# Kernel tuning notes

Hardware: AMD Instinct MI355X
Metric: run time of the kernel (lower is better)

Reference implementation:

```python
import jax, jax.numpy as jnp
import numpy as np
from itertools import product

MAX_ALLOC = [3, 3, 3, 3, 3, 3]   # env.maximum_allocation -> 4^6 = 4096 actions
NUM_SESSIONS = 64
STATE_DIM = NUM_SESSIONS + len(MAX_ALLOC)  # 70
HIDDEN = (1024, 1024)
BATCH = 8192


def setup_inputs() -> dict:
    key = jax.random.key(0)
    ks = jax.random.split(key, 8)
    # states: sessions part uniform [0,1); waitlist part uniform [0,4) so mask is nontrivial
    sessions = jax.random.uniform(ks[0], (BATCH, NUM_SESSIONS), dtype=jnp.float32)
    waitlist = jax.random.uniform(ks[1], (BATCH, len(MAX_ALLOC)), dtype=jnp.float32) * 4.0
    states = jnp.concatenate([sessions, waitlist], axis=1)
    # enumerated action space, same order as itertools.product in the torch module
    action_space = jnp.asarray(
        np.array(list(product(*[range(m + 1) for m in MAX_ALLOC])), dtype=np.int32))  # [4096, 6]
    A = action_space.shape[0]
    W1 = jax.random.normal(ks[2], (STATE_DIM, HIDDEN[0]), dtype=jnp.float32) / np.sqrt(STATE_DIM)
    b1 = jnp.zeros((HIDDEN[0],), dtype=jnp.float32)
    W2 = jax.random.normal(ks[3], (HIDDEN[0], HIDDEN[1]), dtype=jnp.float32) / np.sqrt(HIDDEN[0])
    b2 = jnp.zeros((HIDDEN[1],), dtype=jnp.float32)
    Wh = jax.random.normal(ks[4], (HIDDEN[1], A), dtype=jnp.float32) / np.sqrt(HIDDEN[1])
    bh = jnp.zeros((A,), dtype=jnp.float32)
    return {"states": states, "W1": W1, "b1": b1, "W2": W2, "b2": b2,
            "Wh": Wh, "bh": bh, "action_space": action_space,
            "num_sessions": NUM_SESSIONS}


def reference(states, W1, b1, W2, b2, Wh, bh, action_space, num_sessions):
    # vectorized get_action_mask: action j is feasible for row i iff all(action_j <= waitlist_i)
    waitlist = states[:, num_sessions:]                                   # [B, 6]
    feasible = jnp.all(action_space[None, :, :].astype(states.dtype)
                       <= waitlist[:, None, :], axis=-1)                  # [B, A] bool
    mask = feasible.astype(states.dtype)
    # tanh MLP
    h = jnp.tanh(states @ W1 + b1)
    h = jnp.tanh(h @ W2 + b2)
    logits = h @ Wh + bh + jnp.log(mask + 1e-9)                           # [B, A]
    return jax.nn.softmax(logits, axis=1)
```

## Files before the change

### kernel.cpp

```cpp
#include <hip/hip_runtime.h>
#include <hip/hip_bf16.h>
#include <math.h>

using bf16 = __hip_bfloat16;
typedef __attribute__((ext_vector_type(8))) short short8;
typedef __attribute__((ext_vector_type(4))) float f32x4;
typedef __attribute__((ext_vector_type(4))) unsigned int u32x4;

#define BATCH 8192
#define SDIM  70
#define NS    64
#define HID   1024
#define NA    4096
#define KPAD  128

__device__ __forceinline__ void gld_lds16(const bf16* g, bf16* l) {
    __builtin_amdgcn_global_load_lds(
        (const __attribute__((address_space(1))) void*)g,
        (__attribute__((address_space(3))) void*)l, 16, 0, 0);
}

__device__ __forceinline__ short f2bf(float v) {
    union { bf16 b; short s; } u; u.b = __float2bfloat16(v); return u.s;
}

__device__ __forceinline__ void tr32(const float* __restrict__ in, bf16* __restrict__ out,
                                     int K, int N, int Kpad, int bx, int by, int t,
                                     float (*tile)[33]) {
    int kb = by * 32, nb = bx * 32;
    int tx = t & 31, ty = t >> 5;
    #pragma unroll
    for (int i = 0; i < 32; i += 8) {
        int k = kb + ty + i, n = nb + tx;
        tile[ty + i][tx] = (k < K) ? in[(size_t)k * N + n] : 0.0f;
    }
    __syncthreads();
    #pragma unroll
    for (int i = 0; i < 32; i += 8) {
        int n = nb + ty + i, k = kb + tx;
        if (k < Kpad) out[(size_t)n * Kpad + k] = __float2bfloat16(tile[tx][ty + i]);
    }
}

__global__ __launch_bounds__(256)
void prep_k(const float* __restrict__ states, const float* __restrict__ W1,
            const float* __restrict__ W2, const float* __restrict__ Wh,
            const int* __restrict__ act,
            bf16* __restrict__ statesb, bf16* __restrict__ w1bt,
            bf16* __restrict__ w2bt, bf16* __restrict__ whbt,
            unsigned* __restrict__ pact, unsigned* __restrict__ trow) {
    __shared__ float tile[32][33];
    const int b = blockIdx.x, t = threadIdx.x;
    if (b < 512) {
        int idx = b * 256 + t;
        int row = idx >> 4;
        int c0  = (idx & 15) * 8;
        const float* src = states + (size_t)row * SDIM;
        short8 o;
        #pragma unroll
        for (int i = 0; i < 8; i++) {
            int c = c0 + i;
            o[i] = f2bf((c < SDIM) ? src[c] : 0.0f);
        }
        *(short8*)&statesb[(size_t)row * KPAD + c0] = o;
    } else if (b < 640) {
        int r = b - 512;
        tr32(W1, w1bt, SDIM, HID, KPAD, r & 31, r >> 5, t, tile);
    } else if (b < 1664) {
        int r = b - 640;
        tr32(W2, w2bt, HID, HID, HID, r & 31, r >> 5, t, tile);
    } else if (b < 5760) {
        int r = b - 1664;
        tr32(Wh, whbt, HID, NA, HID, r & 127, r >> 7, t, tile);
    } else if (b < 5776) {
        int c = (b - 5760) * 256 + t;
        if (c < NA) {
            const int* a = act + c * 6;
            unsigned p = 0;
            #pragma unroll
            for (int i = 0; i < 6; i++) p |= ((unsigned)a[i]) << (5 * i);
            pact[c] = p;
        }
    } else {
        int row = (b - 5776) * 256 + t;
        const float* wl = states + (size_t)row * SDIM + NS;
        unsigned T = 0;
        #pragma unroll
        for (int i = 0; i < 6; i++) T |= ((unsigned)(int)wl[i]) << (5 * i);
        trow[row] = T;
    }
}

template<int MODE, int BN>
__global__ __launch_bounds__(256)
void gemm128(const bf16* __restrict__ A, const bf16* __restrict__ BT,
             const float* __restrict__ bias, void* __restrict__ Cout,
             int M, int N, int K,
             const unsigned* __restrict__ trow, const unsigned* __restrict__ pact) {
    const int n0 = blockIdx.x * BN;
    const int m0 = blockIdx.y * 128;
    const int tid  = threadIdx.x;
    const int wave = tid >> 6;
    const int lane = tid & 63;

    constexpr int NJ = BN / 32;
    constexpr int BCH = BN / 8;

    __shared__ __align__(16) bf16 As[128 * 64];
    __shared__ __align__(16) bf16 Bs[BN * 64];

    const int lr = lane >> 3;
    const int gk = ((lane & 7) ^ lr) * 8;
    const bf16* ag = A  + (size_t)(m0 + lr) * K + gk;
    const bf16* bg = BT + (size_t)(n0 + lr) * K + gk;

    f32x4 acc[4][NJ];
    #pragma unroll
    for (int i = 0; i < 4; i++)
        #pragma unroll
        for (int j = 0; j < NJ; j++) acc[i][j] = (f32x4){0.f, 0.f, 0.f, 0.f};

    const int rb = (wave >> 1) * 64;
    const int cb = (wave & 1) * (BN / 2);
    const int fr = lane & 15;
    const int kq = lane >> 4;

    int aoff[2][4], boff[2][NJ];
    #pragma unroll
    for (int kk = 0; kk < 2; kk++) {
        const int cbase = kk * 4 + kq;
        #pragma unroll
        for (int i = 0; i < 4; i++) {
            const int ra = rb + i * 16 + fr;
            aoff[kk][i] = (ra * 64 + ((cbase ^ (fr & 7)) * 8)) * 2;
        }
        #pragma unroll
        for (int j = 0; j < NJ; j++) {
            const int rn = cb + j * 16 + fr;
            boff[kk][j] = (rn * 64 + ((cbase ^ (fr & 7)) * 8)) * 2;
        }
    }
    const char* Asb = (const char*)As;
    const char* Bsb = (const char*)Bs;

    for (int k0 = 0; k0 < K; k0 += 64) {
        #pragma unroll
        for (int q = 0; q < 4; q++) {
            const int ch = q * 4 + wave;
            gld_lds16(ag + (size_t)(ch * 8) * K + k0, &As[ch * 512]);
            if (ch < BCH)
                gld_lds16(bg + (size_t)(ch * 8) * K + k0, &Bs[ch * 512]);
        }
        __syncthreads();

        #pragma unroll
        for (int kk = 0; kk < 2; kk++) {
            short8 af[4], bfr[NJ];
            #pragma unroll
            for (int i = 0; i < 4; i++)  af[i]  = *(const short8*)(Asb + aoff[kk][i]);
            #pragma unroll
            for (int j = 0; j < NJ; j++) bfr[j] = *(const short8*)(Bsb + boff[kk][j]);
            #pragma unroll
            for (int i = 0; i < 4; i++)
                #pragma unroll
                for (int j = 0; j < NJ; j++)
                    acc[i][j] = __builtin_amdgcn_mfma_f32_16x16x32_bf16(af[i], bfr[j], acc[i][j], 0, 0, 0);
        }
        __syncthreads();
    }

    const int orow = m0 + rb + (lane >> 4) * 4;
    const int ocol = n0 + cb + fr;
    float bv[NJ];
    #pragma unroll
    for (int j = 0; j < NJ; j++) bv[j] = bias[ocol + j * 16];
    unsigned pv[NJ];
    if (MODE == 3) {
        #pragma unroll
        for (int j = 0; j < NJ; j++) pv[j] = pact[ocol + j * 16];
    }
    const unsigned H = 0x21084210u;
    #pragma unroll
    for (int i = 0; i < 4; i++) {
        #pragma unroll
        for (int r = 0; r < 4; r++) {
            const int row = orow + i * 16 + r;
            unsigned TH = 0;
            if (MODE == 3) TH = trow[row] | H;
            #pragma unroll
            for (int j = 0; j < NJ; j++) {
                float val = acc[i][j][r] + bv[j];
                const size_t off = (size_t)row * N + ocol + j * 16;
                if (MODE == 0) {
                    ((bf16*)Cout)[off] = __float2bfloat16(tanhf(val));
                } else if (MODE == 1) {
                    ((float*)Cout)[off] = val;
                } else if (MODE == 3) {
                    if (((TH - pv[j]) & H) != H) val -= 20.7232658f;
                    ((bf16*)Cout)[off] = __float2bfloat16(val);
                } else {
                    ((bf16*)Cout)[off] = __float2bfloat16(val);
                }
            }
        }
    }
}

__global__ __launch_bounds__(256)
void softmax_k(const bf16* __restrict__ logitsb, float* __restrict__ out) {
    const int row  = blockIdx.x;
    const int t    = threadIdx.x;
    const int lane = t & 63, wave = t >> 6;

    __shared__ float reds[4];
    __shared__ float ssum;

    const unsigned* lrow = (const unsigned*)(logitsb + (size_t)row * NA) + t * 8;
    u32x4 raw0 = *(const u32x4*)lrow;
    u32x4 raw1 = *(const u32x4*)(lrow + 4);
    unsigned rw[8];
    #pragma unroll
    for (int i = 0; i < 4; i++) { rw[i] = raw0[i]; rw[4 + i] = raw1[i]; }

    float v[16];
    float s = 0.f;
    #pragma unroll
    for (int i = 0; i < 8; i++) {
        float e0 = __expf(__uint_as_float(rw[i] << 16));
        float e1 = __expf(__uint_as_float(rw[i] & 0xffff0000u));
        v[2 * i] = e0; v[2 * i + 1] = e1;
        s += e0 + e1;
    }
    #pragma unroll
    for (int o = 32; o > 0; o >>= 1) s += __shfl_down(s, o, 64);
    if (lane == 0) reds[wave] = s;
    __syncthreads();
    if (t == 0) ssum = reds[0] + reds[1] + reds[2] + reds[3];
    __syncthreads();
    const float inv = 1.0f / ssum;

    float* orow = out + (size_t)row * NA + t * 16;
    #pragma unroll
    for (int q = 0; q < 4; q++) {
        f32x4 o4 = { v[q * 4] * inv, v[q * 4 + 1] * inv,
                     v[q * 4 + 2] * inv, v[q * 4 + 3] * inv };
        *(f32x4*)(orow + q * 4) = o4;
    }
}

extern "C" void kernel_launch(void* const* d_in, const int* in_sizes, int n_in,
                              void* d_out, int out_size, void* d_ws, size_t ws_size,
                              hipStream_t stream) {
    const float* states = (const float*)d_in[0];
    const float* W1 = (const float*)d_in[1];
    const float* b1 = (const float*)d_in[2];
    const float* W2 = (const float*)d_in[3];
    const float* b2 = (const float*)d_in[4];
    const float* Wh = (const float*)d_in[5];
    const float* bh = (const float*)d_in[6];
    const int*   act = (const int*)d_in[7];
    float* out = (float*)d_out;

    char* ws = (char*)d_ws;
    bf16* statesb = (bf16*)ws; ws += (size_t)BATCH * KPAD * 2;
    bf16* w1bt    = (bf16*)ws; ws += (size_t)HID * KPAD * 2;
    bf16* w2bt    = (bf16*)ws; ws += (size_t)HID * HID * 2;
    bf16* whbt    = (bf16*)ws; ws += (size_t)NA * HID * 2;
    bf16* h1      = (bf16*)ws; ws += (size_t)BATCH * HID * 2;
    bf16* h2      = (bf16*)ws; ws += (size_t)BATCH * HID * 2;
    bf16* logitsb = (bf16*)ws; ws += (size_t)BATCH * NA * 2;
    unsigned* pact = (unsigned*)ws; ws += (size_t)NA * 4;
    unsigned* trow = (unsigned*)ws; ws += (size_t)BATCH * 4;

    prep_k<<<5808, 256, 0, stream>>>(states, W1, W2, Wh, act,
                                     statesb, w1bt, w2bt, whbt, pact, trow);

    gemm128<0, 64><<<dim3(HID / 64, BATCH / 128), 256, 0, stream>>>(
        statesb, w1bt, b1, h1, BATCH, HID, KPAD, nullptr, nullptr);
    gemm128<0, 64><<<dim3(HID / 64, BATCH / 128), 256, 0, stream>>>(
        h1, w2bt, b2, h2, BATCH, HID, HID, nullptr, nullptr);
    gemm128<3, 128><<<dim3(NA / 128, BATCH / 128), 256, 0, stream>>>(
        h2, whbt, bh, logitsb, BATCH, NA, HID, trow, pact);

    softmax_k<<<BATCH, 256, 0, stream>>>(logitsb, out);
}
```

Before: 315.1 us.

## Fuse exp and row-sum into head GEMM epilogue, simplify softmax to normalize

Moves the exponentiation and row-sum partial reduction into the final GEMM epilogue, using shuffles and global atomicAdd into a zeroed rowsum buffer. The softmax kernel becomes a pure normalize pass with no block reduction or syncthreads. This removes the exp and reduction work from the last pass but adds 8192x32 atomics. It skips max-subtraction, so it relies on logits staying small enough that exp does not overflow.

```diff
diff --git a/kernel.cpp b/kernel.cpp
--- a/kernel.cpp
+++ b/kernel.cpp
@@ -48,7 +48,8 @@
             const int* __restrict__ act,
             bf16* __restrict__ statesb, bf16* __restrict__ w1bt,
             bf16* __restrict__ w2bt, bf16* __restrict__ whbt,
-            unsigned* __restrict__ pact, unsigned* __restrict__ trow) {
+            unsigned* __restrict__ pact, unsigned* __restrict__ trow,
+            float* __restrict__ rowsum) {
     __shared__ float tile[32][33];
     const int b = blockIdx.x, t = threadIdx.x;
     if (b < 512) {
@@ -81,13 +82,16 @@
             for (int i = 0; i < 6; i++) p |= ((unsigned)a[i]) << (5 * i);
             pact[c] = p;
         }
-    } else {
+    } else if (b < 5808) {
         int row = (b - 5776) * 256 + t;
         const float* wl = states + (size_t)row * SDIM + NS;
         unsigned T = 0;
         #pragma unroll
         for (int i = 0; i < 6; i++) T |= ((unsigned)(int)wl[i]) << (5 * i);
         trow[row] = T;
+    } else {
+        int idx = (b - 5808) * 256 + t;
+        rowsum[idx] = 0.0f;
     }
 }
 
@@ -96,7 +100,8 @@
 void gemm128(const bf16* __restrict__ A, const bf16* __restrict__ BT,
              const float* __restrict__ bias, void* __restrict__ Cout,
              int M, int N, int K,
-             const unsigned* __restrict__ trow, const unsigned* __restrict__ pact) {
+             const unsigned* __restrict__ trow, const unsigned* __restrict__ pact,
+             float* __restrict__ rowsum) {
     const int n0 = blockIdx.x * BN;
     const int m0 = blockIdx.y * 128;
     const int tid  = threadIdx.x;
@@ -187,6 +192,7 @@
             const int row = orow + i * 16 + r;
             unsigned TH = 0;
             if (MODE == 3) TH = trow[row] | H;
+            float rs = 0.f;
             #pragma unroll
             for (int j = 0; j < NJ; j++) {
                 float val = acc[i][j][r] + bv[j];
@@ -197,54 +203,53 @@
                     ((float*)Cout)[off] = val;
                 } else if (MODE == 3) {
                     if (((TH - pv[j]) & H) != H) val -= 20.7232658f;
-                    ((bf16*)Cout)[off] = __float2bfloat16(val);
+                    float e = __expf(val);
+                    ((bf16*)Cout)[off] = __float2bfloat16(e);
+                    rs += e;
                 } else {
                     ((bf16*)Cout)[off] = __float2bfloat16(val);
                 }
             }
+            if (MODE == 3) {
+                rs += __shfl_xor(rs, 1, 64);
+                rs += __shfl_xor(rs, 2, 64);
+                rs += __shfl_xor(rs, 4, 64);
+                rs += __shfl_xor(rs, 8, 64);
+                if (fr == 0) atomicAdd(&rowsum[row], rs);
+            }
         }
     }
 }
 
 __global__ __launch_bounds__(256)
-void softmax_k(const bf16* __restrict__ logitsb, float* __restrict__ out) {
-    const int row  = blockIdx.x;
-    const int t    = threadIdx.x;
-    const int lane = t & 63, wave = t >> 6;
-
-    __shared__ float reds[4];
-    __shared__ float ssum;
-
-    const unsigned* lrow = (const unsigned*)(logitsb + (size_t)row * NA) + t * 8;
+void normalize_k(const bf16* __restrict__ expb, const float* __restrict__ rowsum,
+                 float* __restrict__ out) {
+    const int row = blockIdx.x;
+    const int t   = threadIdx.x;
+
+    const float inv = 1.0f / rowsum[row];
+
+    const unsigned* lrow = (const unsigned*)(expb + (size_t)row * NA) + t * 8;
     u32x4 raw0 = *(const u32x4*)lrow;
     u32x4 raw1 = *(const u32x4*)(lrow + 4);
     unsigned rw[8];
     #pragma unroll
     for (int i = 0; i < 4; i++) { rw[i] = raw0[i]; rw[4 + i] = raw1[i]; }
 
-    float v[16];
-    float s = 0.f;
-    #pragma unroll
-    for (int i = 0; i < 8; i++) {
-        float e0 = __expf(__uint_as_float(rw[i] << 16));
-        float e1 = __expf(__uint_as_float(rw[i] & 0xffff0000u));
-        v[2 * i] = e0; v[2 * i + 1] = e1;
-        s += e0 + e1;
-    }
-    #pragma unroll
-    for (int o = 32; o > 0; o >>= 1) s += __shfl_down(s, o, 64);
-    if (lane == 0) reds[wave] = s;
-    __syncthreads();
-    if (t == 0) ssum = reds[0] + reds[1] + reds[2] + reds[3];
-    __syncthreads();
-    const float inv = 1.0f / ssum;
-
     float* orow = out + (size_t)row * NA + t * 16;
     #pragma unroll
-    for (int q = 0; q < 4; q++) {
-        f32x4 o4 = { v[q * 4] * inv, v[q * 4 + 1] * inv,
-                     v[q * 4 + 2] * inv, v[q * 4 + 3] * inv };
-        *(f32x4*)(orow + q * 4) = o4;
+    for (int q = 0; q < 2; q++) {
+        f32x4 o0, o1;
+        #pragma unroll
+        for (int e = 0; e < 4; e++) {
+            unsigned w = rw[q * 4 + e];
+            float lo = __uint_as_float(w << 16);
+            float hi = __uint_as_float(w & 0xffff0000u);
+            if (e < 2) { o0[2 * e] = lo * inv; o0[2 * e + 1] = hi * inv; }
+            else       { o1[2 * (e - 2)] = lo * inv; o1[2 * (e - 2) + 1] = hi * inv; }
+        }
+        *(f32x4*)(orow + q * 8)     = o0;
+        *(f32x4*)(orow + q * 8 + 4) = o1;
     }
 }
 
@@ -268,19 +273,20 @@
     bf16* whbt    = (bf16*)ws; ws += (size_t)NA * HID * 2;
     bf16* h1      = (bf16*)ws; ws += (size_t)BATCH * HID * 2;
     bf16* h2      = (bf16*)ws; ws += (size_t)BATCH * HID * 2;
-    bf16* logitsb = (bf16*)ws; ws += (size_t)BATCH * NA * 2;
+    bf16* expb    = (bf16*)ws; ws += (size_t)BATCH * NA * 2;
     unsigned* pact = (unsigned*)ws; ws += (size_t)NA * 4;
     unsigned* trow = (unsigned*)ws; ws += (size_t)BATCH * 4;
-
-    prep_k<<<5808, 256, 0, stream>>>(states, W1, W2, Wh, act,
-                                     statesb, w1bt, w2bt, whbt, pact, trow);
+    float* rowsum  = (float*)ws;   ws += (size_t)BATCH * 4;
+
+    prep_k<<<5840, 256, 0, stream>>>(states, W1, W2, Wh, act,
+                                     statesb, w1bt, w2bt, whbt, pact, trow, rowsum);
 
     gemm128<0, 64><<<dim3(HID / 64, BATCH / 128), 256, 0, stream>>>(
-        statesb, w1bt, b1, h1, BATCH, HID, KPAD, nullptr, nullptr);
+        statesb, w1bt, b1, h1, BATCH, HID, KPAD, nullptr, nullptr, nullptr);
     gemm128<0, 64><<<dim3(HID / 64, BATCH / 128), 256, 0, stream>>>(
-        h1, w2bt, b2, h2, BATCH, HID, HID, nullptr, nullptr);
+        h1, w2bt, b2, h2, BATCH, HID, HID, nullptr, nullptr, nullptr);
     gemm128<3, 128><<<dim3(NA / 128, BATCH / 128), 256, 0, stream>>>(
-        h2, whbt, bh, logitsb, BATCH, NA, HID, trow, pact);
-
-    softmax_k<<<BATCH, 256, 0, stream>>>(logitsb, out);
-}
+        h2, whbt, bh, expb, BATCH, NA, HID, trow, pact, rowsum);
+
+    normalize_k<<<BATCH, 256, 0, stream>>>(expb, rowsum, out);
+}
```

New measurement: 327.2 us. 1.04x slower.
